# Optimization experiments

Hardware: AMD Instinct MI355X
Metric: run time of the kernel (lower is better)

Reference implementation:

```python
import jax, jax.numpy as jnp
import numpy as np

B = 16
DRUG_LEN, PROT_LEN = 64, 1200
DIM, CONV = 64, 40


def conv1d(x, w, b):
    # x: [B, C_in, L], w: [C_out, C_in, K] (torch layout), VALID padding
    y = jax.lax.conv_general_dilated(
        x, w, window_strides=(1,), padding='VALID',
        dimension_numbers=('NCH', 'OIH', 'NCH'))
    return y + b[None, :, None]


def setup_inputs() -> dict:
    key = jax.random.key(0)
    ks = jax.random.split(key, 32)
    s = 0.05
    inp = {
        'drug_tokens': jax.random.randint(ks[0], (B, DRUG_LEN), 0, 65, dtype=jnp.int32),
        'protein_tokens': jax.random.randint(ks[1], (B, PROT_LEN), 0, 26, dtype=jnp.int32),
        'drug_emb': (jax.random.normal(ks[2], (65, DIM)) * s).at[0].set(0.0),
        'prot_emb': (jax.random.normal(ks[3], (26, DIM)) * s).at[0].set(0.0),
        'dW1': jax.random.normal(ks[4], (CONV, DIM, 4)) * s,
        'db1': jax.random.normal(ks[5], (CONV,)) * s,
        'dW2': jax.random.normal(ks[6], (CONV * 2, CONV, 6)) * s,
        'db2': jax.random.normal(ks[7], (CONV * 2,)) * s,
        'dW3': jax.random.normal(ks[8], (CONV * 4, CONV * 2, 8)) * s,
        'db3': jax.random.normal(ks[9], (CONV * 4,)) * s,
        'pW1': jax.random.normal(ks[10], (CONV, DIM, 4)) * s,
        'pb1': jax.random.normal(ks[11], (CONV,)) * s,
        'pW2': jax.random.normal(ks[12], (CONV * 2, CONV, 8)) * s,
        'pb2': jax.random.normal(ks[13], (CONV * 2,)) * s,
        'pW3': jax.random.normal(ks[14], (CONV * 4, CONV * 2, 12)) * s,
        'pb3': jax.random.normal(ks[15], (CONV * 4,)) * s,
        'dattW': jax.random.normal(ks[16], (160, 160)) * s,
        'dattb': jax.random.normal(ks[17], (160,)) * s,
        'pattW': jax.random.normal(ks[18], (160, 160)) * s,
        'pattb': jax.random.normal(ks[19], (160,)) * s,
        'attW': jax.random.normal(ks[20], (160, 160)) * s,
        'attb': jax.random.normal(ks[21], (160,)) * s,
        'fc1W': jax.random.normal(ks[22], (1024, 320)) * s,
        'fc1b': jax.random.normal(ks[23], (1024,)) * s,
        'fc2W': jax.random.normal(ks[24], (1024, 1024)) * s,
        'fc2b': jax.random.normal(ks[25], (1024,)) * s,
        'fc3W': jax.random.normal(ks[26], (512, 1024)) * s,
        'fc3b': jax.random.normal(ks[27], (512,)) * s,
        'outW': jax.random.normal(ks[28], (2, 512)) * s,
        'outb': jax.random.normal(ks[29], (2,)) * s,
    }
    return inp


def reference(drug_tokens, protein_tokens, drug_emb, prot_emb,
              dW1, db1, dW2, db2, dW3, db3,
              pW1, pb1, pW2, pb2, pW3, pb3,
              dattW, dattb, pattW, pattb, attW, attb,
              fc1W, fc1b, fc2W, fc2b, fc3W, fc3b, outW, outb):
    relu = jax.nn.relu
    # Embedding lookup, then to [B, C, L]
    de = drug_emb[drug_tokens].transpose(0, 2, 1)    # [B,64,64]
    pe = prot_emb[protein_tokens].transpose(0, 2, 1)  # [B,64,1200]
    # CNN stacks
    dc = relu(conv1d(relu(conv1d(relu(conv1d(de, dW1, db1)), dW2, db2)), dW3, db3))  # [B,160,49]
    pc = relu(conv1d(relu(conv1d(relu(conv1d(pe, pW1, pb1)), pW2, pb2)), pW3, pb3))  # [B,160,1179]
    # Per-token attention projections (Linear over channel dim)
    d_att = jnp.einsum('bcd,oc->bdo', dc, dattW) + dattb   # [B,49,160]
    p_att = jnp.einsum('bcp,oc->bpo', pc, pattW) + pattb   # [B,1179,160]
    # Broadcast outer-sum + ReLU + Linear  -> [B,49,1179,160]
    A = relu(d_att[:, :, None, :] + p_att[:, None, :, :])
    A = jnp.einsum('bdpk,ok->bdpo', A, attW) + attb
    comp_atte = jax.nn.sigmoid(jnp.mean(A, axis=2)).transpose(0, 2, 1)  # [B,160,49]
    prot_atte = jax.nn.sigmoid(jnp.mean(A, axis=1)).transpose(0, 2, 1)  # [B,160,1179]
    dc = dc * 0.5 + dc * comp_atte
    pc = pc * 0.5 + pc * prot_atte
    # Global max pool over length
    dvec = jnp.max(dc, axis=2)  # [B,160]
    pvec = jnp.max(pc, axis=2)  # [B,160]
    pair = jnp.concatenate([dvec, pvec], axis=1)  # [B,320]
    # MLP head (dropout = identity at inference)
    h = jax.nn.leaky_relu(pair @ fc1W.T + fc1b, 0.01)
    h = jax.nn.leaky_relu(h @ fc2W.T + fc2b, 0.01)
    h = jax.nn.leaky_relu(h @ fc3W.T + fc3b, 0.01)
    return h @ outW.T + outb  # [B,2]
```

## Files before the change

### kernel.cpp

```cpp
#include <hip/hip_runtime.h>
#include <hip/hip_bf16.h>

typedef __hip_bfloat16 bf16;
typedef __attribute__((ext_vector_type(8))) short short8;
typedef __attribute__((ext_vector_type(4))) float floatx4;

#define NB 16


__device__ __forceinline__ float b2f(bf16 x) { return __bfloat162float(x); }
__device__ __forceinline__ float u16bf(unsigned short u) {
    return __uint_as_float(((unsigned)u) << 16);
}
__device__ __forceinline__ unsigned short f2bu(float v) {
    union { bf16 h; unsigned short u; } cv;
    cv.h = __float2bfloat16(v);
    return cv.u;
}

__global__ void sniff_kernel(const unsigned short* __restrict__ w, int* __restrict__ flag) {
    __shared__ int cnt;
    if (threadIdx.x == 0) cnt = 0;
    __syncthreads();
    int hits = 0;
    for (int s = 0; s < 4; s++) {
        unsigned short u = w[(threadIdx.x * 4 + s) * 2];
        float v = fabsf(u16bf(u));
        if (v > 1e-6f && v < 2.0f) hits++;
    }
    atomicAdd(&cnt, hits);
    __syncthreads();
    if (threadIdx.x == 0) *flag = (cnt > 512) ? 1 : 0;
}

#define NSEG 14
struct CvtJob {
    const void* src[NSEG];
    float* dst[NSEG];
    int n[NSEG];
};

__global__ void megacvt(CvtJob job, const int* __restrict__ flagp) {
    int seg = blockIdx.y;
    int i = blockIdx.x * 256 + threadIdx.x;
    if (i >= job.n[seg]) return;
    const void* s = job.src[seg];
    if (s == nullptr) { job.dst[seg][i] = 0.f; return; }
    float v = (*flagp) ? b2f(((const bf16*)s)[i]) : ((const float*)s)[i];
    job.dst[seg][i] = v;
}

__global__ void cvt_emb(const void* de, const void* pe, bf16* dB, bf16* pB,
                        const int* __restrict__ flagp) {
    int i = blockIdx.x * 256 + threadIdx.x;
    int f = *flagp;
    if (i < 65 * 64) {
        dB[i] = f ? ((const bf16*)de)[i] : __float2bfloat16(((const float*)de)[i]);
    } else if (i < 65 * 64 + 26 * 64) {
        int j = i - 65 * 64;
        pB[j] = f ? ((const bf16*)pe)[j] : __float2bfloat16(((const float*)pe)[j]);
    }
}

__global__ void pack6(const void* s0, const void* s1, const void* s2,
                      const void* s3, const void* s4, const void* s5,
                      bf16* d0, bf16* d1, bf16* d2, bf16* d3, bf16* d4, bf16* d5,
                      const int* __restrict__ flagp) {
    int y = blockIdx.y;
    const void* src; bf16* dst; int Cout, CIN, K, coP, CIP;
    if (y == 0)      { src = s0; dst = d0; Cout = 40;  CIN = 64; K = 4;  coP = 48;  CIP = 64; }
    else if (y == 1) { src = s1; dst = d1; Cout = 40;  CIN = 64; K = 4;  coP = 48;  CIP = 64; }
    else if (y == 2) { src = s2; dst = d2; Cout = 80;  CIN = 40; K = 6;  coP = 128; CIP = 64; }
    else if (y == 3) { src = s3; dst = d3; Cout = 80;  CIN = 40; K = 8;  coP = 128; CIP = 64; }
    else if (y == 4) { src = s4; dst = d4; Cout = 160; CIN = 80; K = 8;  coP = 192; CIP = 96; }
    else             { src = s5; dst = d5; Cout = 160; CIN = 80; K = 12; coP = 192; CIP = 96; }
    int i = blockIdx.x * 256 + threadIdx.x;
    int total = K * coP * CIP;
    if (i >= total) return;
    int ci = i % CIP;
    int t = i / CIP;
    int co = t % coP;
    int k = t / coP;
    float v = 0.f;
    if (co < Cout && ci < CIN) {
        int s = (co * CIN + ci) * K + k;
        v = (*flagp) ? b2f(((const bf16*)src)[s]) : ((const float*)src)[s];
    }
    dst[i] = __float2bfloat16(v);
}

__global__ void cvt160b(const void* s0, const void* s1, const void* s2,
                        bf16* d0, bf16* d1, bf16* d2, const int* __restrict__ flagp) {
    int i = blockIdx.x * 256 + threadIdx.x;
    if (i >= 25600) return;
    const void* s = blockIdx.y == 0 ? s0 : (blockIdx.y == 1 ? s1 : s2);
    bf16* d = blockIdx.y == 0 ? d0 : (blockIdx.y == 1 ? d1 : d2);
    float v = (*flagp) ? b2f(((const bf16*)s)[i]) : ((const float*)s)[i];
    d[i] = __float2bfloat16(v);
}

template <int K, int CIN, int CHUNKS>
__global__ __launch_bounds__(256) void conv_mfma(const bf16* __restrict__ x,
                                                 const bf16* __restrict__ Wp,
                                                 const float* __restrict__ bias,
                                                 bf16* __restrict__ y,
                                                 int Lin, int Lout, int Cout,
                                                 int coP, int tilesL) {
    const int CIP = CHUNKS * 32;
    const int PCI = CIP + 8;
    const int TLX = 64 + K - 1;
    __shared__ __align__(16) unsigned short xT[TLX * PCI];
    int b = blockIdx.x / tilesL;
    int l0 = (blockIdx.x % tilesL) << 6;
    const unsigned short* xb = (const unsigned short*)x + (size_t)b * CIN * Lin;
    for (int i = threadIdx.x; i < TLX * CIP; i += 256) {
        int ci = i / TLX, l = i - ci * TLX;
        unsigned short v = 0;
        int gl = l0 + l;
        if (ci < CIN && gl < Lin) v = xb[ci * Lin + gl];
        xT[l * PCI + ci] = v;
    }
    __syncthreads();
    int lane = threadIdx.x & 63;
    int w = threadIdx.x >> 6;
    int ct = blockIdx.y * 4 + w;
    int n = lane & 15, quad = lane >> 4;
    floatx4 acc[4];
#pragma unroll
    for (int i = 0; i < 4; i++) acc[i] = (floatx4){0.f, 0.f, 0.f, 0.f};
    const unsigned short* wbase = (const unsigned short*)Wp;
#pragma unroll
    for (int k = 0; k < K; k++) {
#pragma unroll
        for (int ch = 0; ch < CHUNKS; ch++) {
            short8 a = *(const short8*)(wbase +
                        ((size_t)(k * coP + ct * 16 + n)) * CIP + ch * 32 + quad * 8);
#pragma unroll
            for (int nt = 0; nt < 4; nt++) {
                short8 bb = *(const short8*)(xT + (nt * 16 + n + k) * PCI + ch * 32 + quad * 8);
                acc[nt] = __builtin_amdgcn_mfma_f32_16x16x32_bf16(a, bb, acc[nt], 0, 0, 0);
            }
        }
    }
    int m0 = quad * 4;
#pragma unroll
    for (int nt = 0; nt < 4; nt++) {
        int l = l0 + nt * 16 + n;
        if (l >= Lout) continue;
#pragma unroll
        for (int r = 0; r < 4; r++) {
            int co = ct * 16 + m0 + r;
            if (co < Cout)
                y[((size_t)b * Cout + co) * Lout + l] =
                    __float2bfloat16(fmaxf(acc[nt][r] + bias[co], 0.f));
        }
    }
}

__global__ __launch_bounds__(256) void conv1_mfma(const int* __restrict__ dtok,
                                                  const int* __restrict__ ptok,
                                                  const bf16* __restrict__ embDB,
                                                  const bf16* __restrict__ embPB,
                                                  const bf16* __restrict__ dW1p,
                                                  const bf16* __restrict__ pW1p,
                                                  const float* __restrict__ db1f,
                                                  const float* __restrict__ pb1f,
                                                  bf16* __restrict__ d1,
                                                  bf16* __restrict__ p1) {
    const int K = 4, CIP = 64, PCI = 72, TLX = 67, coP = 48, Cout = 40;
    __shared__ __align__(16) unsigned short xT[TLX * PCI];
    __shared__ int stok[TLX];
    bool isD = blockIdx.x < 16;
    int b, l0, Lin, Lout;
    const int* tok; const unsigned short* embB; const unsigned short* Wp;
    const float* bias; bf16* y;
    if (isD) {
        b = blockIdx.x; l0 = 0; Lin = 64; Lout = 61;
        tok = dtok; embB = (const unsigned short*)embDB;
        Wp = (const unsigned short*)dW1p; bias = db1f; y = d1;
    } else {
        int bx = blockIdx.x - 16;
        b = bx / 19; l0 = (bx % 19) << 6; Lin = 1200; Lout = 1197;
        tok = ptok; embB = (const unsigned short*)embPB;
        Wp = (const unsigned short*)pW1p; bias = pb1f; y = p1;
    }
    if (threadIdx.x < TLX) {
        int l = l0 + threadIdx.x;
        stok[threadIdx.x] = (l < Lin) ? tok[b * Lin + l] : -1;
    }
    __syncthreads();
    for (int i = threadIdx.x; i < TLX * CIP; i += 256) {
        int ci = i / TLX, l = i - ci * TLX;
        int t = stok[l];
        xT[l * PCI + ci] = (t >= 0) ? embB[t * 64 + ci] : (unsigned short)0;
    }
    __syncthreads();
    int lane = threadIdx.x & 63;
    int w = threadIdx.x >> 6;
    int n = lane & 15, quad = lane >> 4;
    if (w >= 3) return;
    floatx4 acc[4];
#pragma unroll
    for (int i = 0; i < 4; i++) acc[i] = (floatx4){0.f, 0.f, 0.f, 0.f};
#pragma unroll
    for (int k = 0; k < K; k++) {
#pragma unroll
        for (int ch = 0; ch < 2; ch++) {
            short8 a = *(const short8*)(Wp +
                        ((size_t)(k * coP + w * 16 + n)) * CIP + ch * 32 + quad * 8);
#pragma unroll
            for (int nt = 0; nt < 4; nt++) {
                short8 bb = *(const short8*)(xT + (nt * 16 + n + k) * PCI + ch * 32 + quad * 8);
                acc[nt] = __builtin_amdgcn_mfma_f32_16x16x32_bf16(a, bb, acc[nt], 0, 0, 0);
            }
        }
    }
    int m0 = quad * 4;
#pragma unroll
    for (int nt = 0; nt < 4; nt++) {
        int l = l0 + nt * 16 + n;
        if (l >= Lout) continue;
#pragma unroll
        for (int r = 0; r < 4; r++) {
            int co = w * 16 + m0 + r;
            if (co < Cout)
                y[((size_t)b * Cout + co) * Lout + l] =
                    __float2bfloat16(fmaxf(acc[nt][r] + bias[co], 0.f));
        }
    }
}

__global__ __launch_bounds__(256) void att_proj_mfma(const bf16* __restrict__ dcB,
                                                     const bf16* __restrict__ pcB,
                                                     const bf16* __restrict__ dWB,
                                                     const bf16* __restrict__ pWB,
                                                     const float* __restrict__ dbF,
                                                     const float* __restrict__ pbF,
                                                     float* __restrict__ datt,
                                                     bf16* __restrict__ pattB) {
    const int PCI = 168;
    __shared__ __align__(16) unsigned short xT[64 * PCI];
    bool isD = blockIdx.x < 16;
    int b, l0, L;
    const unsigned short* xsrc; const unsigned short* W; const float* bias;
    if (isD) {
        b = blockIdx.x; l0 = 0; L = 49;
        xsrc = (const unsigned short*)dcB; W = (const unsigned short*)dWB; bias = dbF;
    } else {
        int bx = blockIdx.x - 16;
        b = bx / 19; l0 = (bx % 19) << 6; L = 1179;
        xsrc = (const unsigned short*)pcB; W = (const unsigned short*)pWB; bias = pbF;
    }
    const unsigned short* xb = xsrc + (size_t)b * 160 * L;
    for (int i = threadIdx.x; i < 160 * 64; i += 256) {
        int c = i >> 6, j = i & 63;
        int l = l0 + j;
        xT[j * PCI + c] = (l < L) ? xb[(size_t)c * L + l] : (unsigned short)0;
    }
    __syncthreads();
    int lane = threadIdx.x & 63;
    int w = threadIdx.x >> 6;
    int t = blockIdx.y * 4 + w;
    int n = lane & 15, quad = lane >> 4;
    if (t >= 10) return;
    floatx4 acc[4];
#pragma unroll
    for (int i = 0; i < 4; i++) acc[i] = (floatx4){0.f, 0.f, 0.f, 0.f};
#pragma unroll
    for (int ch = 0; ch < 5; ch++) {
        short8 a = *(const short8*)(W + ((size_t)(t * 16 + n)) * 160 + ch * 32 + quad * 8);
#pragma unroll
        for (int nt = 0; nt < 4; nt++) {
            short8 bb = *(const short8*)(xT + (nt * 16 + n) * PCI + ch * 32 + quad * 8);
            acc[nt] = __builtin_amdgcn_mfma_f32_16x16x32_bf16(a, bb, acc[nt], 0, 0, 0);
        }
    }
    int m0 = quad * 4;
    int o0 = t * 16 + m0;
#pragma unroll
    for (int nt = 0; nt < 4; nt++) {
        int l = l0 + nt * 16 + n;
        if (l >= L) continue;
        if (isD) {
            float4 v;
            v.x = acc[nt][0] + bias[o0 + 0];
            v.y = acc[nt][1] + bias[o0 + 1];
            v.z = acc[nt][2] + bias[o0 + 2];
            v.w = acc[nt][3] + bias[o0 + 3];
            *(float4*)(datt + ((size_t)b * 49 + l) * 160 + o0) = v;
        } else {
            ushort4 u;
            u.x = f2bu(acc[nt][0] + bias[o0 + 0]);
            u.y = f2bu(acc[nt][1] + bias[o0 + 1]);
            u.z = f2bu(acc[nt][2] + bias[o0 + 2]);
            u.w = f2bu(acc[nt][3] + bias[o0 + 3]);
            *(ushort4*)((unsigned short*)pattB + ((size_t)b * 1179 + l) * 160 + o0) = u;
        }
    }
}

__global__ __launch_bounds__(320) void mean_fused(const float* __restrict__ datt,
                                                  const bf16* __restrict__ patt,
                                                  bf16* __restrict__ MpW,
                                                  float* __restrict__ Mdpart) {
    __shared__ __align__(16) unsigned short sp[37 * 160];
    int tid = threadIdx.x;
    int b = blockIdx.x >> 5;
    int pc = blockIdx.x & 31;
    int p0 = pc * 37;
    int pmax = 1179 - p0;
    if (pmax > 37) pmax = 37;
    {
        const short8* src = (const short8*)((const unsigned short*)patt +
                                            ((size_t)b * 1179 + p0) * 160);
        short8* dst = (short8*)sp;
        int n8 = (pmax * 160) >> 3;
        for (int v = tid; v < n8; v += 320) dst[v] = src[v];
    }
    int h = tid & 1;
    int k = tid >> 1;
    int d0 = h ? 25 : 0;
    int nd = h ? 24 : 25;
    const float* drow = datt + (size_t)b * 49 * 160 + k;
    float dv[25], md[25];
#pragma unroll
    for (int i = 0; i < 25; i++) {
        dv[i] = (i < nd) ? drow[(d0 + i) * 160] : -1e30f;
        md[i] = 0.f;
    }
    __syncthreads();
    unsigned short* mp = (unsigned short*)MpW + ((size_t)b * 1184 + p0) * 160 + k;
#pragma unroll 2
    for (int pi = 0; pi < pmax; pi++) {
        float pv = u16bf(sp[pi * 160 + k]);
        float s0 = 0.f, s1 = 0.f, s2 = 0.f, s3 = 0.f, s4 = 0.f;
#pragma unroll
        for (int g = 0; g < 5; g++) {
            float r0 = fmaxf(dv[g * 5 + 0] + pv, 0.f);
            float r1 = fmaxf(dv[g * 5 + 1] + pv, 0.f);
            float r2 = fmaxf(dv[g * 5 + 2] + pv, 0.f);
            float r3 = fmaxf(dv[g * 5 + 3] + pv, 0.f);
            float r4 = fmaxf(dv[g * 5 + 4] + pv, 0.f);
            md[g * 5 + 0] += r0; s0 += r0;
            md[g * 5 + 1] += r1; s1 += r1;
            md[g * 5 + 2] += r2; s2 += r2;
            md[g * 5 + 3] += r3; s3 += r3;
            md[g * 5 + 4] += r4; s4 += r4;
        }
        float s = ((s0 + s1) + (s2 + s3)) + s4;
        s += __shfl_xor(s, 1, 64);
        if (h == 0) mp[(size_t)pi * 160] = f2bu(s * (1.f / 49.f));
    }
    float* op = Mdpart + (((size_t)b * 32 + pc) * 49) * 160 + k;
#pragma unroll
    for (int i = 0; i < 25; i++)
        if (i < nd) op[(d0 + i) * 160] = md[i];
}

__global__ __launch_bounds__(256) void md_reduce(const float* __restrict__ Mdpart,
                                                 float* __restrict__ Md) {
    int i = blockIdx.x * 256 + threadIdx.x;
    if (i >= NB * 49 * 160) return;
    int b = i / (49 * 160);
    int dk = i - b * (49 * 160);
    const float* src = Mdpart + (size_t)b * 32 * 49 * 160 + dk;
    float s0 = 0.f, s1 = 0.f, s2 = 0.f, s3 = 0.f;
#pragma unroll
    for (int pc = 0; pc < 32; pc += 4) {
        s0 += src[(size_t)(pc + 0) * 49 * 160];
        s1 += src[(size_t)(pc + 1) * 49 * 160];
        s2 += src[(size_t)(pc + 2) * 49 * 160];
        s3 += src[(size_t)(pc + 3) * 49 * 160];
    }
    Md[i] = (s0 + s1) + (s2 + s3);
}

__global__ __launch_bounds__(256) void att_sig_mfma(const float* __restrict__ Md,
                                                    const bf16* __restrict__ MpW,
                                                    const bf16* __restrict__ wattB,
                                                    const float* __restrict__ attbF,
                                                    const bf16* __restrict__ dcB,
                                                    const bf16* __restrict__ pcB,
                                                    float* __restrict__ pair) {
    const int PCI = 168;
    __shared__ __align__(16) unsigned short sM[64 * PCI];
    bool isD = blockIdx.x < 16;
    int b, p0, L, off;
    const unsigned short* conv;
    if (isD) {
        b = blockIdx.x; p0 = 0; L = 49; off = 0; conv = (const unsigned short*)dcB;
        for (int i = threadIdx.x; i < 160 * 64; i += 256) {
            int r = i / 160, k = i - r * 160;
            float v = (r < 49) ? Md[((size_t)b * 49 + r) * 160 + k] * (1.f / 1179.f) : 0.f;
            sM[r * PCI + k] = f2bu(v);
        }
    } else {
        int bx = blockIdx.x - 16;
        b = bx / 19; p0 = (bx % 19) << 6; L = 1179; off = 160;
        conv = (const unsigned short*)pcB;
        const unsigned short* mb = (const unsigned short*)MpW + (size_t)b * 1184 * 160;
        for (int i = threadIdx.x; i < 160 * 64; i += 256) {
            int r = i / 160, k = i - r * 160;
            int p = p0 + r;
            sM[r * PCI + k] = (p < 1179) ? mb[(size_t)p * 160 + k] : (unsigned short)0;
        }
    }
    __syncthreads();
    int lane = threadIdx.x & 63;
    int w = threadIdx.x >> 6;
    int t = blockIdx.y * 4 + w;
    int n = lane & 15, quad = lane >> 4;
    if (t >= 10) return;
    floatx4 acc[4];
#pragma unroll
    for (int i = 0; i < 4; i++) acc[i] = (floatx4){0.f, 0.f, 0.f, 0.f};
    const unsigned short* W = (const unsigned short*)wattB;
#pragma unroll
    for (int ch = 0; ch < 5; ch++) {
        short8 a = *(const short8*)(W + ((size_t)(t * 16 + n)) * 160 + ch * 32 + quad * 8);
#pragma unroll
        for (int nt = 0; nt < 4; nt++) {
            short8 bb = *(const short8*)(sM + (nt * 16 + n) * PCI + ch * 32 + quad * 8);
            acc[nt] = __builtin_amdgcn_mfma_f32_16x16x32_bf16(a, bb, acc[nt], 0, 0, 0);
        }
    }
    int m0 = quad * 4;
    float vmax[4] = {0.f, 0.f, 0.f, 0.f};
#pragma unroll
    for (int nt = 0; nt < 4; nt++) {
        int p = p0 + nt * 16 + n;
#pragma unroll
        for (int r = 0; r < 4; r++) {
            int o = t * 16 + m0 + r;
            float sig = 1.f / (1.f + __expf(-(acc[nt][r] + attbF[o])));
            float v = 0.f;
            if (p < L) v = u16bf(conv[((size_t)b * 160 + o) * L + p]) * (0.5f + sig);
            vmax[r] = fmaxf(vmax[r], v);
        }
    }
#pragma unroll
    for (int m = 1; m < 16; m <<= 1) {
#pragma unroll
        for (int r = 0; r < 4; r++)
            vmax[r] = fmaxf(vmax[r], __shfl_xor(vmax[r], m, 64));
    }
    if (n == 0) {
#pragma unroll
        for (int r = 0; r < 4; r++)
            atomicMax((unsigned int*)(pair + b * 320 + off + t * 16 + m0 + r),
                      __float_as_uint(vmax[r]));
    }
}

__global__ __launch_bounds__(256) void fc_block(const float* __restrict__ in,
                                                const void* __restrict__ W,
                                                const float* __restrict__ bias,
                                                float* __restrict__ out,
                                                int IN, int OUT,
                                                const int* __restrict__ flagp) {
    int j = blockIdx.x;
    int w = threadIdx.x >> 6, li = threadIdx.x & 63;
    int nv = IN >> 2;
    const float4* i0 = (const float4*)(in + (size_t)(w * 4 + 0) * IN);
    const float4* i1 = (const float4*)(in + (size_t)(w * 4 + 1) * IN);
    const float4* i2 = (const float4*)(in + (size_t)(w * 4 + 2) * IN);
    const float4* i3 = (const float4*)(in + (size_t)(w * 4 + 3) * IN);
    float p0 = 0.f, p1 = 0.f, p2 = 0.f, p3 = 0.f;
    if (*flagp) {
        const ushort4* w4 = (const ushort4*)((const unsigned short*)W + (size_t)j * IN);
        for (int v = li; v < nv; v += 64) {
            ushort4 u = w4[v];
            float wa = u16bf(u.x), wb = u16bf(u.y), wc = u16bf(u.z), wd = u16bf(u.w);
            float4 x;
            x = i0[v]; p0 += x.x * wa + x.y * wb + x.z * wc + x.w * wd;
            x = i1[v]; p1 += x.x * wa + x.y * wb + x.z * wc + x.w * wd;
            x = i2[v]; p2 += x.x * wa + x.y * wb + x.z * wc + x.w * wd;
            x = i3[v]; p3 += x.x * wa + x.y * wb + x.z * wc + x.w * wd;
        }
    } else {
        const float4* w4 = (const float4*)((const float*)W + (size_t)j * IN);
        for (int v = li; v < nv; v += 64) {
            float4 u = w4[v];
            float4 x;
            x = i0[v]; p0 += x.x * u.x + x.y * u.y + x.z * u.z + x.w * u.w;
            x = i1[v]; p1 += x.x * u.x + x.y * u.y + x.z * u.z + x.w * u.w;
            x = i2[v]; p2 += x.x * u.x + x.y * u.y + x.z * u.z + x.w * u.w;
            x = i3[v]; p3 += x.x * u.x + x.y * u.y + x.z * u.z + x.w * u.w;
        }
    }
#pragma unroll
    for (int m = 1; m < 64; m <<= 1) {
        p0 += __shfl_xor(p0, m, 64);
        p1 += __shfl_xor(p1, m, 64);
        p2 += __shfl_xor(p2, m, 64);
        p3 += __shfl_xor(p3, m, 64);
    }
    if (li == 0) {
        float bj = bias[j];
        float o0 = p0 + bj, o1 = p1 + bj, o2 = p2 + bj, o3 = p3 + bj;
        o0 = o0 > 0.f ? o0 : 0.01f * o0;
        o1 = o1 > 0.f ? o1 : 0.01f * o1;
        o2 = o2 > 0.f ? o2 : 0.01f * o2;
        o3 = o3 > 0.f ? o3 : 0.01f * o3;
        out[(size_t)(w * 4 + 0) * OUT + j] = o0;
        out[(size_t)(w * 4 + 1) * OUT + j] = o1;
        out[(size_t)(w * 4 + 2) * OUT + j] = o2;
        out[(size_t)(w * 4 + 3) * OUT + j] = o3;
    }
}

__global__ __launch_bounds__(256) void out_block(const float* __restrict__ h,
                                                 const void* __restrict__ W,
                                                 const float* __restrict__ biasF,
                                                 void* __restrict__ out,
                                                 const int* __restrict__ flagp) {
    int j = blockIdx.x;
    int w = threadIdx.x >> 6, li = threadIdx.x & 63;
    const int IN = 512, nv = 128;
    const float4* i0 = (const float4*)(h + (size_t)(w * 4 + 0) * IN);
    const float4* i1 = (const float4*)(h + (size_t)(w * 4 + 1) * IN);
    const float4* i2 = (const float4*)(h + (size_t)(w * 4 + 2) * IN);
    const float4* i3 = (const float4*)(h + (size_t)(w * 4 + 3) * IN);
    float p0 = 0.f, p1 = 0.f, p2 = 0.f, p3 = 0.f;
    int flag = *flagp;
    if (flag) {
        const ushort4* w4 = (const ushort4*)((const unsigned short*)W + (size_t)j * IN);
        for (int v = li; v < nv; v += 64) {
            ushort4 u = w4[v];
            float wa = u16bf(u.x), wb = u16bf(u.y), wc = u16bf(u.z), wd = u16bf(u.w);
            float4 x;
            x = i0[v]; p0 += x.x * wa + x.y * wb + x.z * wc + x.w * wd;
            x = i1[v]; p1 += x.x * wa + x.y * wb + x.z * wc + x.w * wd;
            x = i2[v]; p2 += x.x * wa + x.y * wb + x.z * wc + x.w * wd;
            x = i3[v]; p3 += x.x * wa + x.y * wb + x.z * wc + x.w * wd;
        }
    } else {
        const float4* w4 = (const float4*)((const float*)W + (size_t)j * IN);
        for (int v = li; v < nv; v += 64) {
            float4 u = w4[v];
            float4 x;
            x = i0[v]; p0 += x.x * u.x + x.y * u.y + x.z * u.z + x.w * u.w;
            x = i1[v]; p1 += x.x * u.x + x.y * u.y + x.z * u.z + x.w * u.w;
            x = i2[v]; p2 += x.x * u.x + x.y * u.y + x.z * u.z + x.w * u.w;
            x = i3[v]; p3 += x.x * u.x + x.y * u.y + x.z * u.z + x.w * u.w;
        }
    }
#pragma unroll
    for (int m = 1; m < 64; m <<= 1) {
        p0 += __shfl_xor(p0, m, 64);
        p1 += __shfl_xor(p1, m, 64);
        p2 += __shfl_xor(p2, m, 64);
        p3 += __shfl_xor(p3, m, 64);
    }
    if (li == 0) {
        float bj = biasF[j];
        float o0 = p0 + bj, o1 = p1 + bj, o2 = p2 + bj, o3 = p3 + bj;
        if (flag) {
            bf16* ob = (bf16*)out;
            ob[(w * 4 + 0) * 2 + j] = __float2bfloat16(o0);
            ob[(w * 4 + 1) * 2 + j] = __float2bfloat16(o1);
            ob[(w * 4 + 2) * 2 + j] = __float2bfloat16(o2);
            ob[(w * 4 + 3) * 2 + j] = __float2bfloat16(o3);
        } else {
            float* of = (float*)out;
            of[(w * 4 + 0) * 2 + j] = o0;
            of[(w * 4 + 1) * 2 + j] = o1;
            of[(w * 4 + 2) * 2 + j] = o2;
            of[(w * 4 + 3) * 2 + j] = o3;
        }
    }
}

extern "C" void kernel_launch(void* const* d_in, const int* in_sizes, int n_in,
                              void* d_out, int out_size, void* d_ws, size_t ws_size,
                              hipStream_t stream) {
    const int* drug_tok = (const int*)d_in[0];
    const int* prot_tok = (const int*)d_in[1];
    const void* drug_emb = d_in[2];
    const void* prot_emb = d_in[3];
    const void* dW1 = d_in[4];  const void* db1 = d_in[5];
    const void* dW2 = d_in[6];  const void* db2 = d_in[7];
    const void* dW3 = d_in[8];  const void* db3 = d_in[9];
    const void* pW1 = d_in[10]; const void* pb1 = d_in[11];
    const void* pW2 = d_in[12]; const void* pb2 = d_in[13];
    const void* pW3 = d_in[14]; const void* pb3 = d_in[15];
    const void* dattW = d_in[16]; const void* dattb = d_in[17];
    const void* pattW = d_in[18]; const void* pattb = d_in[19];
    const void* attW  = d_in[20]; const void* attb  = d_in[21];
    const void* fc1W = d_in[22]; const void* fc1b = d_in[23];
    const void* fc2W = d_in[24]; const void* fc2b = d_in[25];
    const void* fc3W = d_in[26]; const void* fc3b = d_in[27];
    const void* outW = d_in[28]; const void* outb = d_in[29];

    char* base = (char*)d_ws;
    size_t cur = 0;
    auto alloc = [&](size_t bytes) -> char* {
        char* p = base + cur;
        cur = (cur + bytes + 255) & ~(size_t)255;
        return p;
    };
    int*   flag  = (int*)alloc(256);
    bf16* embDB = (bf16*)alloc(65 * 64 * 2);
    bf16* embPB = (bf16*)alloc(26 * 64 * 2);
    bf16* dW1p = (bf16*)alloc((size_t)4 * 48 * 64 * 2);
    bf16* pW1p = (bf16*)alloc((size_t)4 * 48 * 64 * 2);
    bf16* dW2p = (bf16*)alloc((size_t)6 * 128 * 64 * 2);
    bf16* dW3p = (bf16*)alloc((size_t)8 * 192 * 96 * 2);
    bf16* pW2p = (bf16*)alloc((size_t)8 * 128 * 64 * 2);
    bf16* pW3p = (bf16*)alloc((size_t)12 * 192 * 96 * 2);
    float* db1f = (float*)alloc(40 * 4);
    float* db2f = (float*)alloc(80 * 4);
    float* db3f = (float*)alloc(160 * 4);
    float* pb1f = (float*)alloc(40 * 4);
    float* pb2f = (float*)alloc(80 * 4);
    float* pb3f = (float*)alloc(160 * 4);
    float* dattbF = (float*)alloc(160 * 4);
    float* pattbF = (float*)alloc(160 * 4);
    float* attbF  = (float*)alloc(160 * 4);
    float* fc1bF = (float*)alloc(1024 * 4);
    float* fc2bF = (float*)alloc(1024 * 4);
    float* fc3bF = (float*)alloc(512 * 4);
    float* outbF = (float*)alloc(2 * 4);
    bf16* dattWB = (bf16*)alloc(25600 * 2);
    bf16* pattWB = (bf16*)alloc(25600 * 2);
    bf16* wattB  = (bf16*)alloc(25600 * 2);
    bf16* d1  = (bf16*)alloc((size_t)NB * 40 * 61 * 2);
    bf16* d2  = (bf16*)alloc((size_t)NB * 80 * 56 * 2);
    bf16* dcB = (bf16*)alloc((size_t)NB * 160 * 49 * 2);
    bf16* p1  = (bf16*)alloc((size_t)NB * 40 * 1197 * 2);
    bf16* p2  = (bf16*)alloc((size_t)NB * 80 * 1190 * 2);
    bf16* pcB = (bf16*)alloc((size_t)NB * 160 * 1179 * 2);
    float* datt  = (float*)alloc((size_t)NB * 49 * 160 * 4);
    bf16* pattB = (bf16*)alloc((size_t)NB * 1179 * 160 * 2);
    float* Md   = (float*)alloc((size_t)NB * 49 * 160 * 4);
    float* Mdpart = (float*)alloc((size_t)NB * 32 * 49 * 160 * 4);
    bf16* MpW  = (bf16*)alloc((size_t)NB * 1184 * 160 * 2);
    float* pair = (float*)alloc(NB * 320 * 4);
    float* h1 = (float*)alloc(NB * 1024 * 4);
    float* h2 = (float*)alloc(NB * 1024 * 4);
    float* h3 = (float*)alloc(NB * 512 * 4);

    sniff_kernel<<<1, 256, 0, stream>>>((const unsigned short*)fc2W, flag);

    CvtJob job;
    int si = 0;
    auto add = [&](const void* s, float* d, int n) { job.src[si] = s; job.dst[si] = d; job.n[si] = n; si++; };
    add(db1, db1f, 40); add(db2, db2f, 80); add(db3, db3f, 160);
    add(pb1, pb1f, 40); add(pb2, pb2f, 80); add(pb3, pb3f, 160);
    add(dattb, dattbF, 160); add(pattb, pattbF, 160); add(attb, attbF, 160);
    add(fc1b, fc1bF, 1024); add(fc2b, fc2bF, 1024); add(fc3b, fc3bF, 512);
    add(outb, outbF, 2);
    add(nullptr, pair, NB * 320);
    megacvt<<<dim3(20, NSEG), 256, 0, stream>>>(job, flag);
    cvt_emb<<<23, 256, 0, stream>>>(drug_emb, prot_emb, embDB, embPB, flag);
    pack6<<<dim3(864, 6), 256, 0, stream>>>(dW1, pW1, dW2, pW2, dW3, pW3,
                                            dW1p, pW1p, dW2p, pW2p, dW3p, pW3p, flag);
    cvt160b<<<dim3(100, 3), 256, 0, stream>>>(dattW, pattW, attW, dattWB, pattWB, wattB, flag);

    conv1_mfma<<<16 + 16 * 19, 256, 0, stream>>>(drug_tok, prot_tok, embDB, embPB,
                                                 dW1p, pW1p, db1f, pb1f, d1, p1);
    conv_mfma<6, 40, 2><<<dim3(16, 2), 256, 0, stream>>>(d1, dW2p, db2f, d2, 61, 56, 80, 128, 1);
    conv_mfma<8, 40, 2><<<dim3(16 * 19, 2), 256, 0, stream>>>(p1, pW2p, pb2f, p2, 1197, 1190, 80, 128, 19);
    conv_mfma<8, 80, 3><<<dim3(16, 3), 256, 0, stream>>>(d2, dW3p, db3f, dcB, 56, 49, 160, 192, 1);
    conv_mfma<12, 80, 3><<<dim3(16 * 19, 3), 256, 0, stream>>>(p2, pW3p, pb3f, pcB, 1190, 1179, 160, 192, 19);

    att_proj_mfma<<<dim3(16 + 304, 3), 256, 0, stream>>>(dcB, pcB, dattWB, pattWB,
                                                         dattbF, pattbF, datt, pattB);

    mean_fused<<<16 * 32, 320, 0, stream>>>(datt, pattB, MpW, Mdpart);
    md_reduce<<<490, 256, 0, stream>>>(Mdpart, Md);

    att_sig_mfma<<<dim3(16 + 304, 3), 256, 0, stream>>>(Md, MpW, wattB, attbF, dcB, pcB, pair);

    fc_block<<<1024, 256, 0, stream>>>(pair, fc1W, fc1bF, h1, 320, 1024, flag);
    fc_block<<<1024, 256, 0, stream>>>(h1, fc2W, fc2bF, h2, 1024, 1024, flag);
    fc_block<<<512, 256, 0, stream>>>(h2, fc3W, fc3bF, h3, 1024, 512, flag);
    out_block<<<2, 256, 0, stream>>>(h3, outW, outbF, d_out, flag);
}
```

Measured before the change: 279.4 us.

## Merge prep and conv launches, split mean_fused drug rows across four threads

Three small conversion kernels (embedding cast, conv weight pack, 160x160 weight cast) become one table-driven packN launch. The drug and protein conv2 and conv3 launches are each merged into a single dual-branch kernel. mean_fused now runs 640 threads per block, with each channel's 49 drug rows split four ways and a second shuffle for the reduction. The aim is fewer launches and more parallelism and fewer registers per thread in the dominant outer-sum mean kernel, at the cost of extra shuffles and heavier blocks.

Measured after the change: 251.8 us. -9.9%, faster.

```diff
diff --git a/kernel.cpp b/kernel.cpp
--- a/kernel.cpp
+++ b/kernel.cpp
@@ -50,30 +50,19 @@
     job.dst[seg][i] = v;
 }
 
-__global__ void cvt_emb(const void* de, const void* pe, bf16* dB, bf16* pB,
-                        const int* __restrict__ flagp) {
-    int i = blockIdx.x * 256 + threadIdx.x;
-    int f = *flagp;
-    if (i < 65 * 64) {
-        dB[i] = f ? ((const bf16*)de)[i] : __float2bfloat16(((const float*)de)[i]);
-    } else if (i < 65 * 64 + 26 * 64) {
-        int j = i - 65 * 64;
-        pB[j] = f ? ((const bf16*)pe)[j] : __float2bfloat16(((const float*)pe)[j]);
-    }
-}
-
-__global__ void pack6(const void* s0, const void* s1, const void* s2,
-                      const void* s3, const void* s4, const void* s5,
-                      bf16* d0, bf16* d1, bf16* d2, bf16* d3, bf16* d4, bf16* d5,
-                      const int* __restrict__ flagp) {
+#define NPK 11
+struct PackJob {
+    const void* src[NPK];
+    bf16* dst[NPK];
+    short Cout[NPK], CIN[NPK], K[NPK], coP[NPK], CIP[NPK];
+};
+
+__global__ void packN(PackJob job, const int* __restrict__ flagp) {
     int y = blockIdx.y;
-    const void* src; bf16* dst; int Cout, CIN, K, coP, CIP;
-    if (y == 0)      { src = s0; dst = d0; Cout = 40;  CIN = 64; K = 4;  coP = 48;  CIP = 64; }
-    else if (y == 1) { src = s1; dst = d1; Cout = 40;  CIN = 64; K = 4;  coP = 48;  CIP = 64; }
-    else if (y == 2) { src = s2; dst = d2; Cout = 80;  CIN = 40; K = 6;  coP = 128; CIP = 64; }
-    else if (y == 3) { src = s3; dst = d3; Cout = 80;  CIN = 40; K = 8;  coP = 128; CIP = 64; }
-    else if (y == 4) { src = s4; dst = d4; Cout = 160; CIN = 80; K = 8;  coP = 192; CIP = 96; }
-    else             { src = s5; dst = d5; Cout = 160; CIN = 80; K = 12; coP = 192; CIP = 96; }
+    int Cout = job.Cout[y], CIN = job.CIN[y], K = job.K[y];
+    int coP = job.coP[y], CIP = job.CIP[y];
+    const void* src = job.src[y];
+    bf16* dst = job.dst[y];
     int i = blockIdx.x * 256 + threadIdx.x;
     int total = K * coP * CIP;
     if (i >= total) return;
@@ -89,30 +78,17 @@
     dst[i] = __float2bfloat16(v);
 }
 
-__global__ void cvt160b(const void* s0, const void* s1, const void* s2,
-                        bf16* d0, bf16* d1, bf16* d2, const int* __restrict__ flagp) {
-    int i = blockIdx.x * 256 + threadIdx.x;
-    if (i >= 25600) return;
-    const void* s = blockIdx.y == 0 ? s0 : (blockIdx.y == 1 ? s1 : s2);
-    bf16* d = blockIdx.y == 0 ? d0 : (blockIdx.y == 1 ? d1 : d2);
-    float v = (*flagp) ? b2f(((const bf16*)s)[i]) : ((const float*)s)[i];
-    d[i] = __float2bfloat16(v);
-}
-
 template <int K, int CIN, int CHUNKS>
-__global__ __launch_bounds__(256) void conv_mfma(const bf16* __restrict__ x,
-                                                 const bf16* __restrict__ Wp,
-                                                 const float* __restrict__ bias,
-                                                 bf16* __restrict__ y,
-                                                 int Lin, int Lout, int Cout,
-                                                 int coP, int tilesL) {
+__device__ __forceinline__ void conv_body(unsigned short* xT,
+                                          const unsigned short* xb,
+                                          const unsigned short* wbase,
+                                          const float* __restrict__ bias,
+                                          bf16* __restrict__ y,
+                                          int b, int Lin, int Lout,
+                                          int Cout, int coP, int l0) {
     const int CIP = CHUNKS * 32;
     const int PCI = CIP + 8;
     const int TLX = 64 + K - 1;
-    __shared__ __align__(16) unsigned short xT[TLX * PCI];
-    int b = blockIdx.x / tilesL;
-    int l0 = (blockIdx.x % tilesL) << 6;
-    const unsigned short* xb = (const unsigned short*)x + (size_t)b * CIN * Lin;
     for (int i = threadIdx.x; i < TLX * CIP; i += 256) {
         int ci = i / TLX, l = i - ci * TLX;
         unsigned short v = 0;
@@ -128,7 +104,6 @@
     floatx4 acc[4];
 #pragma unroll
     for (int i = 0; i < 4; i++) acc[i] = (floatx4){0.f, 0.f, 0.f, 0.f};
-    const unsigned short* wbase = (const unsigned short*)Wp;
 #pragma unroll
     for (int k = 0; k < K; k++) {
 #pragma unroll
@@ -154,6 +129,34 @@
                 y[((size_t)b * Cout + co) * Lout + l] =
                     __float2bfloat16(fmaxf(acc[nt][r] + bias[co], 0.f));
         }
+    }
+}
+
+template <int KD, int KP, int CIN, int CHUNKS>
+__global__ __launch_bounds__(256) void conv_dual(const bf16* __restrict__ xd,
+                                                 const bf16* __restrict__ Wpd,
+                                                 const float* __restrict__ bd,
+                                                 bf16* __restrict__ yd, int LinD, int LoutD,
+                                                 const bf16* __restrict__ xp,
+                                                 const bf16* __restrict__ Wpp,
+                                                 const float* __restrict__ bp,
+                                                 bf16* __restrict__ yp, int LinP, int LoutP,
+                                                 int Cout, int coP) {
+    const int CIP = CHUNKS * 32;
+    const int PCI = CIP + 8;
+    const int TLXMAX = 64 + KP - 1;
+    __shared__ __align__(16) unsigned short xT[TLXMAX * PCI];
+    if (blockIdx.x < 16) {
+        int b = blockIdx.x;
+        conv_body<KD, CIN, CHUNKS>(xT, (const unsigned short*)xd + (size_t)b * CIN * LinD,
+                                   (const unsigned short*)Wpd, bd, yd, b, LinD, LoutD,
+                                   Cout, coP, 0);
+    } else {
+        int bx = blockIdx.x - 16;
+        int b = bx / 19, l0 = (bx % 19) << 6;
+        conv_body<KP, CIN, CHUNKS>(xT, (const unsigned short*)xp + (size_t)b * CIN * LinP,
+                                   (const unsigned short*)Wpp, bp, yp, b, LinP, LoutP,
+                                   Cout, coP, l0);
     }
 }
 
@@ -299,7 +302,7 @@
     }
 }
 
-__global__ __launch_bounds__(320) void mean_fused(const float* __restrict__ datt,
+__global__ __launch_bounds__(640) void mean_fused(const float* __restrict__ datt,
                                                   const bf16* __restrict__ patt,
                                                   bf16* __restrict__ MpW,
                                                   float* __restrict__ Mdpart) {
@@ -315,16 +318,16 @@
                                             ((size_t)b * 1179 + p0) * 160);
         short8* dst = (short8*)sp;
         int n8 = (pmax * 160) >> 3;
-        for (int v = tid; v < n8; v += 320) dst[v] = src[v];
-    }
-    int h = tid & 1;
-    int k = tid >> 1;
-    int d0 = h ? 25 : 0;
-    int nd = h ? 24 : 25;
+        for (int v = tid; v < n8; v += 640) dst[v] = src[v];
+    }
+    int h = tid & 3;
+    int k = tid >> 2;
+    int d0 = h * 13;
+    int nd = (h == 3) ? 10 : 13;
     const float* drow = datt + (size_t)b * 49 * 160 + k;
-    float dv[25], md[25];
-#pragma unroll
-    for (int i = 0; i < 25; i++) {
+    float dv[13], md[13];
+#pragma unroll
+    for (int i = 0; i < 13; i++) {
         dv[i] = (i < nd) ? drow[(d0 + i) * 160] : -1e30f;
         md[i] = 0.f;
     }
@@ -333,27 +336,30 @@
 #pragma unroll 2
     for (int pi = 0; pi < pmax; pi++) {
         float pv = u16bf(sp[pi * 160 + k]);
-        float s0 = 0.f, s1 = 0.f, s2 = 0.f, s3 = 0.f, s4 = 0.f;
-#pragma unroll
-        for (int g = 0; g < 5; g++) {
-            float r0 = fmaxf(dv[g * 5 + 0] + pv, 0.f);
-            float r1 = fmaxf(dv[g * 5 + 1] + pv, 0.f);
-            float r2 = fmaxf(dv[g * 5 + 2] + pv, 0.f);
-            float r3 = fmaxf(dv[g * 5 + 3] + pv, 0.f);
-            float r4 = fmaxf(dv[g * 5 + 4] + pv, 0.f);
-            md[g * 5 + 0] += r0; s0 += r0;
-            md[g * 5 + 1] += r1; s1 += r1;
-            md[g * 5 + 2] += r2; s2 += r2;
-            md[g * 5 + 3] += r3; s3 += r3;
-            md[g * 5 + 4] += r4; s4 += r4;
-        }
-        float s = ((s0 + s1) + (s2 + s3)) + s4;
+        float s0 = 0.f, s1 = 0.f, s2 = 0.f, s3 = 0.f;
+#pragma unroll
+        for (int g = 0; g < 3; g++) {
+            float r0 = fmaxf(dv[g * 4 + 0] + pv, 0.f);
+            float r1 = fmaxf(dv[g * 4 + 1] + pv, 0.f);
+            float r2 = fmaxf(dv[g * 4 + 2] + pv, 0.f);
+            float r3 = fmaxf(dv[g * 4 + 3] + pv, 0.f);
+            md[g * 4 + 0] += r0; s0 += r0;
+            md[g * 4 + 1] += r1; s1 += r1;
+            md[g * 4 + 2] += r2; s2 += r2;
+            md[g * 4 + 3] += r3; s3 += r3;
+        }
+        {
+            float r = fmaxf(dv[12] + pv, 0.f);
+            md[12] += r; s0 += r;
+        }
+        float s = (s0 + s1) + (s2 + s3);
         s += __shfl_xor(s, 1, 64);
+        s += __shfl_xor(s, 2, 64);
         if (h == 0) mp[(size_t)pi * 160] = f2bu(s * (1.f / 49.f));
     }
     float* op = Mdpart + (((size_t)b * 32 + pc) * 49) * 160 + k;
 #pragma unroll
-    for (int i = 0; i < 25; i++)
+    for (int i = 0; i < 13; i++)
         if (i < nd) op[(d0 + i) * 160] = md[i];
 }
 
@@ -652,22 +658,40 @@
     add(outb, outbF, 2);
     add(nullptr, pair, NB * 320);
     megacvt<<<dim3(20, NSEG), 256, 0, stream>>>(job, flag);
-    cvt_emb<<<23, 256, 0, stream>>>(drug_emb, prot_emb, embDB, embPB, flag);
-    pack6<<<dim3(864, 6), 256, 0, stream>>>(dW1, pW1, dW2, pW2, dW3, pW3,
-                                            dW1p, pW1p, dW2p, pW2p, dW3p, pW3p, flag);
-    cvt160b<<<dim3(100, 3), 256, 0, stream>>>(dattW, pattW, attW, dattWB, pattWB, wattB, flag);
+
+    PackJob pj;
+    int pi = 0;
+    auto seg = [&](const void* s, bf16* d, int Cout, int CIN, int K, int coP, int CIP) {
+        pj.src[pi] = s; pj.dst[pi] = d;
+        pj.Cout[pi] = Cout; pj.CIN[pi] = CIN; pj.K[pi] = K; pj.coP[pi] = coP; pj.CIP[pi] = CIP;
+        pi++;
+    };
+    seg(dW1, dW1p, 40, 64, 4, 48, 64);
+    seg(pW1, pW1p, 40, 64, 4, 48, 64);
+    seg(dW2, dW2p, 80, 40, 6, 128, 64);
+    seg(pW2, pW2p, 80, 40, 8, 128, 64);
+    seg(dW3, dW3p, 160, 80, 8, 192, 96);
+    seg(pW3, pW3p, 160, 80, 12, 192, 96);
+    seg(dattW, dattWB, 160, 160, 1, 160, 160);
+    seg(pattW, pattWB, 160, 160, 1, 160, 160);
+    seg(attW,  wattB,  160, 160, 1, 160, 160);
+    seg(drug_emb, embDB, 65, 64, 1, 65, 64);
+    seg(prot_emb, embPB, 26, 64, 1, 26, 64);
+    packN<<<dim3(864, NPK), 256, 0, stream>>>(pj, flag);
 
     conv1_mfma<<<16 + 16 * 19, 256, 0, stream>>>(drug_tok, prot_tok, embDB, embPB,
                                                  dW1p, pW1p, db1f, pb1f, d1, p1);
-    conv_mfma<6, 40, 2><<<dim3(16, 2), 256, 0, stream>>>(d1, dW2p, db2f, d2, 61, 56, 80, 128, 1);
-    conv_mfma<8, 40, 2><<<dim3(16 * 19, 2), 256, 0, stream>>>(p1, pW2p, pb2f, p2, 1197, 1190, 80, 128, 19);
-    conv_mfma<8, 80, 3><<<dim3(16, 3), 256, 0, stream>>>(d2, dW3p, db3f, dcB, 56, 49, 160, 192, 1);
-    conv_mfma<12, 80, 3><<<dim3(16 * 19, 3), 256, 0, stream>>>(p2, pW3p, pb3f, pcB, 1190, 1179, 160, 192, 19);
+    conv_dual<6, 8, 40, 2><<<dim3(16 + 304, 2), 256, 0, stream>>>(
+        d1, dW2p, db2f, d2, 61, 56,
+        p1, pW2p, pb2f, p2, 1197, 1190, 80, 128);
+    conv_dual<8, 12, 80, 3><<<dim3(16 + 304, 3), 256, 0, stream>>>(
+        d2, dW3p, db3f, dcB, 56, 49,
+        p2, pW3p, pb3f, pcB, 1190, 1179, 160, 192);
 
     att_proj_mfma<<<dim3(16 + 304, 3), 256, 0, stream>>>(dcB, pcB, dattWB, pattWB,
                                                          dattbF, pattbF, datt, pattB);
 
-    mean_fused<<<16 * 32, 320, 0, stream>>>(datt, pattB, MpW, Mdpart);
+    mean_fused<<<16 * 32, 640, 0, stream>>>(datt, pattB, MpW, Mdpart);
     md_reduce<<<490, 256, 0, stream>>>(Mdpart, Md);
 
     att_sig_mfma<<<dim3(16 + 304, 3), 256, 0, stream>>>(Md, MpW, wattB, attbF, dcB, pcB, pair);
```
